# Kernel optimization log

Hardware: AMD Instinct MI355X
Metric: run time of the kernel (lower is better)

The kernel has to match this reference:

```python
import jax, jax.numpy as jnp
import numpy as np
from jax import lax

B, T, D, V, K = 32, 2048, 512, 1024, 3
COVERAGE_FLOOR = 0.05
LN_EPS = 1e-5


def _gelu(x):
    return jax.nn.gelu(x, approximate=False)  # torch F.gelu default is exact erf


def _causal_conv(h, w, b):
    # h: [B,T,D]; w: [D_out, D_in, K]; left-pad (K-1) for causality
    x = jnp.transpose(h, (0, 2, 1))  # [B,D,T]
    y = lax.conv_general_dilated(x, w, window_strides=(1,),
                                 padding=[(w.shape[-1] - 1, 0)],
                                 dimension_numbers=("NCH", "OIH", "NCH"))
    return jnp.transpose(y + b[None, :, None], (0, 2, 1))  # [B,T,D]


def _layer_norm(x, g, b):
    m = x.mean(-1, keepdims=True)
    v = ((x - m) ** 2).mean(-1, keepdims=True)
    return (x - m) / jnp.sqrt(v + LN_EPS) * g + b


def _masked_median(values, mask):
    # values, mask: [B,T]; torch median = lower middle = sorted[(n-1)//2]
    valid = mask > 0.5
    n = valid.sum(axis=1)  # [B]
    s = jnp.sort(jnp.where(valid, values, jnp.inf), axis=1)
    idx = jnp.clip((n - 1) // 2, 0, values.shape[1] - 1)
    med = jnp.take_along_axis(s, idx[:, None], axis=1)  # [B,1]
    return jnp.where((n > 0)[:, None], med, 0.0)


def _masked_mean(values, mask):
    denom = jnp.clip(mask.sum(axis=1, keepdims=True), 1.0, None)  # [B,1]
    return (values * mask[:, :, None]).sum(axis=1) / denom  # [B,D]


def _masked_std(values, mask, mean):
    denom = jnp.clip(mask.sum(axis=1, keepdims=True), 1.0, None)
    diff2 = (values - mean[:, None, :]) ** 2 * mask[:, :, None]
    return jnp.sqrt(diff2.sum(axis=1) / jnp.clip(denom, 1e-6, None) + 1e-6)


def setup_inputs() -> dict:
    key = jax.random.key(0)
    ks = jax.random.split(key, 16)
    s = 0.02
    return {
        "unit_ids": jax.random.randint(ks[0], (B, T), 0, V),
        "duration_obs": jax.random.uniform(ks[1], (B, T), jnp.float32, 0.01, 2.0),
        "mask": (jax.random.uniform(ks[2], (B, T)) > 0.3).astype(jnp.float32),
        "emb": jax.random.normal(ks[3], (V, D), jnp.float32) * s,
        "aux_w": jax.random.normal(ks[4], (D, 1), jnp.float32) * s,
        "aux_b": jnp.zeros((D,), jnp.float32),
        "conv1_w": jax.random.normal(ks[5], (D, D, K), jnp.float32) * s,
        "conv1_b": jnp.zeros((D,), jnp.float32),
        "conv2_w": jax.random.normal(ks[6], (D, D, K), jnp.float32) * s,
        "conv2_b": jnp.zeros((D,), jnp.float32),
        "ln_g": jnp.ones((D,), jnp.float32),
        "ln_b": jnp.zeros((D,), jnp.float32),
        "p1_w": jax.random.normal(ks[7], (D, 2 * D), jnp.float32) * s,
        "p1_b": jnp.zeros((D,), jnp.float32),
        "p2_w": jax.random.normal(ks[8], (D, D), jnp.float32) * s,
        "p2_b": jnp.zeros((D,), jnp.float32),
    }


def reference(unit_ids, duration_obs, mask, emb, aux_w, aux_b,
              conv1_w, conv1_b, conv2_w, conv2_b, ln_g, ln_b,
              p1_w, p1_b, p2_w, p2_b):
    mask = jnp.clip(mask.astype(jnp.float32), 0.0, 1.0)  # [B,T]
    logdur = jnp.log(jnp.clip(duration_obs.astype(jnp.float32), 1e-4, None)) * mask
    global_rate = _masked_median(logdur, mask)  # [B,1]
    ref_residual = (logdur - global_rate) * mask  # [B,T]

    # CausalStretchQueryEncoder
    hidden = emb[unit_ids] + (ref_residual[:, :, None] * aux_w[None, None, :, 0] + aux_b)
    hidden = _gelu(_causal_conv(hidden, conv1_w, conv1_b))
    hidden = _gelu(_causal_conv(hidden, conv2_w, conv2_b))
    hidden = _layer_norm(hidden, ln_g, ln_b) * mask[:, :, None]  # [B,T,D]

    mean = _masked_mean(hidden, mask)  # [B,D]
    std = _masked_std(hidden, mask, mean)  # [B,D]
    h = jnp.concatenate([mean, std], axis=-1)  # [B,2D]
    summary_state = jnp.tanh(_gelu(h @ p1_w.T + p1_b) @ p2_w.T + p2_b)  # [B,D]

    support_raw = mask.sum(axis=1, keepdims=True)  # [B,1]
    support = jnp.clip(support_raw, 1.0, None)
    summary_state = jnp.where(support_raw > 0.0, summary_state, 0.0)
    coverage = jnp.clip(support_raw / float(T), COVERAGE_FLOOR, None)

    residual_mean = (ref_residual * mask).sum(axis=1, keepdims=True) / support  # [B,1]
    residual_var = jnp.clip(((ref_residual - residual_mean) ** 2 * mask).sum(axis=1, keepdims=True) / support, 1e-4, None)
    attn = (mask / support)[:, :, None]  # [B,T,1]
    prompt_role_fit = residual_mean * jnp.ones_like(ref_residual) * mask  # [B,T]
    coeff_norm = jnp.linalg.norm(summary_state, axis=-1, keepdims=True)  # [B,1]

    return (global_rate, summary_state, residual_mean, residual_var, coverage,
            mask, logdur, ref_residual, attn, prompt_role_fit, coeff_norm)
```

## Files before the change

kernel.cpp:

```cpp
#include <hip/hip_runtime.h>
#include <hip/hip_bf16.h>
#include <math.h>

#define B_  32
#define T_  2048
#define D_  512
#define V_  1024
#define K_  3

typedef __attribute__((ext_vector_type(8))) short   short8;
typedef __attribute__((ext_vector_type(4))) float   floatx4;
typedef __attribute__((ext_vector_type(2))) long    longx2;

#define SCALE_H0 256.0f
#define SCALE_A  64.0f
#define SCALE_W  16.0f
#define INV1 (1.0f/(SCALE_H0*SCALE_W))
#define INV2 (1.0f/(SCALE_A*SCALE_W))

#define OFF0 0
#define OFF1 32
#define OFF2 16416
#define OFF3 16448
#define OFF4 16480
#define OFF5 16512
#define OFF6 82048
#define OFF7 147584
#define OFF8 213120
#define OFF9 278656
#define OFF10 344192

#define WS_RR     0
#define WS_SUP    262144
#define WS_PSUM   262272
#define WS_PSUMSQ 327808
#define WS_W1P    393344
#define WS_W2P    1212544
#define WS_H1     2031744
#define WS_S1     35618944
#define WS_NRM    35684480

__device__ __forceinline__ float clampf(float v, float lo, float hi) {
    v = (v > lo) ? v : lo;
    return (v < hi) ? v : hi;
}
__device__ __forceinline__ float gelu_exact(float v) {
    return 0.5f * v * (1.0f + erff(v * 0.70710678118654752440f));
}
__device__ __forceinline__ unsigned char f2fp8(float x) {
    int v = __builtin_amdgcn_cvt_pk_fp8_f32(x, x, 0, false);
    return (unsigned char)(v & 0xFF);
}
__device__ __forceinline__ int pk4fp8(float a, float b, float c, float d) {
    int p0 = __builtin_amdgcn_cvt_pk_fp8_f32(a, b, 0, false);
    int p1 = __builtin_amdgcn_cvt_pk_fp8_f32(c, d, 0, false);
    return (p1 << 16) | (p0 & 0xFFFF);
}

__device__ __forceinline__ float block_reduce_sum(float v, float* red, int tid) {
    __syncthreads();
    red[tid] = v;
    __syncthreads();
    for (int s = 128; s > 0; s >>= 1) {
        if (tid < s) red[tid] += red[tid + s];
        __syncthreads();
    }
    float r = red[0];
    __syncthreads();
    return r;
}

#define NB 2048
#define HLO (-9.3f)
#define HSC ((float)NB / 10.05f)
#define WLS 1544
__global__ __launch_bounds__(256) void init_kernel(
    const float* __restrict__ dur, const float* __restrict__ maskp,
    const float* __restrict__ w1, const float* __restrict__ w2,
    unsigned char* __restrict__ W1p, unsigned char* __restrict__ W2p,
    unsigned char* __restrict__ H1buf,
    float* __restrict__ rr_ws, float* __restrict__ sup_ws,
    float* __restrict__ psum, float* __restrict__ out)
{
    int tid = threadIdx.x;

    if (blockIdx.x >= 32) {
        __shared__ unsigned char Wl[2 * 16 * WLS];
        int ntg = blockIdx.x - 32;
        int lane = tid & 63, wave = tid >> 6;

        #pragma unroll
        for (int ws = 0; ws < 2; ++ws) {
            const float* wsrc = (ws ? w2 : w1) + (size_t)ntg * 16 * 1536;
            for (int i = tid; i < 6144; i += 256) {
                float4 v = ((const float4*)wsrc)[i];
                int col_local = i / 384;
                int pos = (i % 384) * 4;
                int word = pk4fp8(v.x * SCALE_W, v.y * SCALE_W,
                                  v.z * SCALE_W, v.w * SCALE_W);
                *(int*)(&Wl[(ws * 16 + col_local) * WLS + pos]) = word;
            }
        }
        __syncthreads();

        int cl = lane & 15, qq = lane >> 4;
        int pg = ntg >> 1, half = ntg & 1;
        #pragma unroll
        for (int ws = 0; ws < 2; ++ws) {
            unsigned char* dst = ws ? W2p : W1p;
            for (int s = wave; s < 48; s += 4) {
                int ci = s & 15, k = s >> 4;
                const unsigned char* row = &Wl[(ws * 16 + cl) * WLS];
                int kin = ci * 32 + qq * 8;
                unsigned char bb[8];
                #pragma unroll
                for (int e = 0; e < 8; ++e)
                    bb[e] = row[(kin + e) * 3 + k];
                *(double*)(dst + (((size_t)(s * 16 + pg) * 64 + lane) * 16
                                  + half * 8)) = *(double*)bb;
            }
        }

        int pid2 = ntg * 256 + tid;
        #pragma unroll
        for (int j = 0; j < 4; ++j) {
            int idx = pid2 + j * 8192;
            psum[idx] = 0.0f;
            int b = idx >> 10;
            int r = (idx >> 9) & 1;
            int d = idx & 511;
            H1buf[((size_t)b * 2050 + r) * 512 + d] = 0;
        }
        return;
    }

    __shared__ int   hist[NB];
    __shared__ int   csum[256];
    __shared__ float red[256];
    __shared__ float cand[128];
    __shared__ float nsh, medsh;
    __shared__ int   sh_tb, sh_cb, sh_candn;

    int b = blockIdx.x;
    const float* durb = dur + (size_t)b * T_;
    const float* mkb  = maskp + (size_t)b * T_;

    float ld[8], mk[8];
    int   bn[8];
    float cnt = 0.0f;
    #pragma unroll
    for (int i = 0; i < 8; ++i) hist[tid * 8 + i] = 0;
    __syncthreads();
    #pragma unroll
    for (int i = 0; i < 8; ++i) {
        int t = tid + i * 256;
        float m = clampf(mkb[t], 0.0f, 1.0f);
        float dv = durb[t];
        dv = (dv >= 1e-4f) ? dv : 1e-4f;
        float l = logf(dv) * m;
        ld[i] = l; mk[i] = m;
        int bin = (int)((l - HLO) * HSC);
        bin = (bin < 0) ? 0 : ((bin > NB - 1) ? NB - 1 : bin);
        bn[i] = bin;
        if (m > 0.5f) { cnt += 1.0f; atomicAdd(&hist[bin], 1); }
    }
    float n = block_reduce_sum(cnt, red, tid);
    if (tid == 0) { nsh = n; sh_candn = 0; medsh = 0.0f; }

    {
        int cs = 0;
        #pragma unroll
        for (int i = 0; i < 8; ++i) cs += hist[tid * 8 + i];
        csum[tid] = cs;
        __syncthreads();
        for (int off = 1; off < 256; off <<= 1) {
            int v = (tid >= off) ? csum[tid - off] : 0;
            __syncthreads();
            csum[tid] += v;
            __syncthreads();
        }
    }
    int ni = (int)(n + 0.5f);
    int k  = (ni > 0) ? ((ni - 1) >> 1) : 0;
    {
        int prevIncl = (tid > 0) ? csum[tid - 1] : 0;
        if (ni > 0 && k >= prevIncl && k < csum[tid]) {
            int cum = prevIncl, tb = tid * 8;
            #pragma unroll
            for (int i = 0; i < 8; ++i) {
                int c = hist[tid * 8 + i];
                if (k < cum + c) { tb = tid * 8 + i; break; }
                cum += c;
            }
            sh_tb = tb; sh_cb = cum;
        }
    }
    __syncthreads();
    if (ni > 0) {
        int tb = sh_tb;
        #pragma unroll
        for (int i = 0; i < 8; ++i) {
            if (mk[i] > 0.5f && bn[i] == tb) {
                int p = atomicAdd(&sh_candn, 1);
                if (p < 128) cand[p] = ld[i];
            }
        }
    }
    __syncthreads();
    if (tid == 0 && ni > 0) {
        int m = k - sh_cb;
        int cn = (sh_candn < 128) ? sh_candn : 128;
        float best = cand[0];
        for (int i = 0; i < cn; ++i) {
            int rank = 0;
            for (int j = 0; j < cn; ++j)
                rank += (cand[j] < cand[i]) || (cand[j] == cand[i] && j < i);
            if (rank == m) { best = cand[i]; break; }
        }
        medsh = best;
    }
    __syncthreads();
    float med = (ni > 0) ? medsh : 0.0f;
    med = clampf(med, -20.0f, 20.0f);

    float denom = (n > 1.0f) ? n : 1.0f;
    float rv[8];
    float ssum = 0.0f;
    #pragma unroll
    for (int i = 0; i < 8; ++i) { rv[i] = (ld[i] - med) * mk[i]; ssum += rv[i]; }
    float rsum = block_reduce_sum(ssum, red, tid);
    float rm = clampf(rsum / denom, -40.0f, 40.0f);

    float vsum_l = 0.0f;
    #pragma unroll
    for (int i = 0; i < 8; ++i) { float dd = rv[i] - rm; vsum_l += dd * dd * mk[i]; }
    float vsum = block_reduce_sum(vsum_l, red, tid);
    float var = clampf(vsum / denom, 1e-4f, 1e4f);

    float inv_sup = 1.0f / denom;
    #pragma unroll
    for (int i = 0; i < 8; ++i) {
        int t = tid + i * 256;
        size_t o = (size_t)b * T_ + t;
        out[OFF5 + o] = mk[i];
        out[OFF6 + o] = ld[i];
        out[OFF7 + o] = rv[i];
        out[OFF8 + o] = mk[i] * inv_sup;
        out[OFF9 + o] = rm * mk[i];
        rr_ws[o] = rv[i];
    }
    if (tid == 0) {
        out[OFF0 + b] = med;
        out[OFF2 + b] = rm;
        out[OFF3 + b] = var;
        float cov = n * (1.0f / (float)T_);
        out[OFF4 + b] = (cov > 0.05f) ? cov : 0.05f;
        sup_ws[b] = n;
    }
}

#define H0S 520
__global__ __launch_bounds__(256, 3) void conv1g_kernel(
    const int* __restrict__ ids, const float* __restrict__ rr,
    const float* __restrict__ emb,
    const float* __restrict__ aux_w, const float* __restrict__ aux_b,
    const unsigned char* __restrict__ W1p, const float* __restrict__ bias1,
    unsigned char* __restrict__ H1buf)
{
    __shared__ __align__(16) unsigned char H0s[66 * H0S];
    __shared__ int   lid[66];
    __shared__ float lrr[66];

    int tile = blockIdx.x;
    int b    = blockIdx.y;
    int r0   = tile << 6;
    int tid  = threadIdx.x;
    int wave = tid >> 6, lane = tid & 63;
    int q = lane >> 4, m16 = lane & 15;

    if (tid < 66) {
        int t = r0 - 2 + tid;
        bool v = (t >= 0);
        lid[tid] = v ? ids[b * T_ + t] : -1;
        lrr[tid] = v ? rr[(size_t)b * T_ + t] : 0.0f;
    }
    __syncthreads();

    {
        int c4 = tid & 127;
        float4 aw = *(const float4*)(aux_w + c4 * 4);
        float4 ab = *(const float4*)(aux_b + c4 * 4);
        int rbase = tid >> 7;
        for (int j = 0; j < 33; ++j) {
            int row = rbase + j * 2;
            int id = lid[row];
            int word = 0;
            if (id >= 0) {
                float vr = lrr[row];
                float4 e = *(const float4*)(emb + (size_t)id * D_ + c4 * 4);
                word = pk4fp8((e.x + vr * aw.x + ab.x) * SCALE_H0,
                              (e.y + vr * aw.y + ab.y) * SCALE_H0,
                              (e.z + vr * aw.z + ab.z) * SCALE_H0,
                              (e.w + vr * aw.w + ab.w) * SCALE_H0);
            }
            *(int*)(&H0s[row * H0S + c4 * 4]) = word;
        }
    }
    __syncthreads();

    unsigned char* Ob = H1buf + ((size_t)b * 2050 + 2 + r0) * 512;

#define CONV1_PHASE(FR0, FR1, SS)                                              \
    {   int k1 = (SS) >> 4, ci = (SS) & 15;                                    \
        _Pragma("unroll")                                                      \
        for (int mt = 0; mt < 4; ++mt) {                                       \
            long afr = *(const long*)(&H0s[(mt * 16 + m16 + k1) * H0S + ci * 32 + q * 8]); \
            acc[mt][0] = __builtin_amdgcn_mfma_f32_16x16x32_fp8_fp8(afr, FR0[0], acc[mt][0], 0, 0, 0); \
            acc[mt][1] = __builtin_amdgcn_mfma_f32_16x16x32_fp8_fp8(afr, FR0[1], acc[mt][1], 0, 0, 0); \
            acc[mt][2] = __builtin_amdgcn_mfma_f32_16x16x32_fp8_fp8(afr, FR1[0], acc[mt][2], 0, 0, 0); \
            acc[mt][3] = __builtin_amdgcn_mfma_f32_16x16x32_fp8_fp8(afr, FR1[1], acc[mt][3], 0, 0, 0); \
        } }

    #pragma unroll
    for (int nh = 0; nh < 2; ++nh) {
        floatx4 acc[4][4];
        #pragma unroll
        for (int i = 0; i < 4; ++i)
            #pragma unroll
            for (int j = 0; j < 4; ++j)
                acc[i][j] = (floatx4){0.f, 0.f, 0.f, 0.f};

        const longx2* wp0 = (const longx2*)W1p
                          + ((size_t)(0 * 16 + nh * 8 + wave * 2 + 0) * 64 + lane);
        const longx2* wp1 = wp0 + 64;

        longx2 fA0 = wp0[0],                  fA1 = wp1[0];
        longx2 fB0 = wp0[(size_t)1 * 1024],   fB1 = wp1[(size_t)1 * 1024];
        longx2 fC0, fC1, fD0, fD1;

        #pragma unroll 1
        for (int s = 0; s < 48; s += 4) {
            fC0 = wp0[(size_t)(s + 2) * 1024]; fC1 = wp1[(size_t)(s + 2) * 1024];
            CONV1_PHASE(fA0, fA1, s)
            fD0 = wp0[(size_t)(s + 3) * 1024]; fD1 = wp1[(size_t)(s + 3) * 1024];
            CONV1_PHASE(fB0, fB1, s + 1)
            fA0 = wp0[(size_t)(s + 4) * 1024]; fA1 = wp1[(size_t)(s + 4) * 1024];
            CONV1_PHASE(fC0, fC1, s + 2)
            fB0 = wp0[(size_t)(s + 5) * 1024]; fB1 = wp1[(size_t)(s + 5) * 1024];
            CONV1_PHASE(fD0, fD1, s + 3)
        }

        #pragma unroll
        for (int mt = 0; mt < 4; ++mt) {
            #pragma unroll
            for (int nt = 0; nt < 4; ++nt) {
                int col = nh * 256 + wave * 64 + nt * 16 + m16;
                float bsv = bias1[col];
                #pragma unroll
                for (int r = 0; r < 4; ++r) {
                    int row = mt * 16 + q * 4 + r;
                    float v = gelu_exact(acc[mt][nt][r] * INV1 + bsv) * SCALE_A;
                    Ob[(size_t)row * 512 + col] = f2fp8(v);
                }
            }
        }
    }
#undef CONV1_PHASE
}

#define H1S 520
__global__ __launch_bounds__(256, 2) void conv2ln_kernel(
    const unsigned char* __restrict__ H1buf, const unsigned char* __restrict__ W2p,
    const float* __restrict__ bias2,
    const float* __restrict__ ln_g, const float* __restrict__ ln_b,
    const float* __restrict__ maskp,
    float* __restrict__ psum, float* __restrict__ psumsq)
{
    __shared__ __align__(16) unsigned char H1s[34 * H1S];
    __shared__ float mrow[32];
    __shared__ float part[32][4][2];
    __shared__ float tot[32][2];
    __shared__ float colsum[512][2];

    int tile = blockIdx.x;
    int b    = blockIdx.y;
    int r0   = tile << 5;
    int tid  = threadIdx.x;
    int wave = tid >> 6, lane = tid & 63;
    int q = lane >> 4, m16 = lane & 15;
    int nbase = wave << 7;

    const unsigned char* src = H1buf + ((size_t)b * 2050 + r0) * 512;
    for (int g = tid; g < 34 * 32; g += 256) {
        int row = g >> 5, h = g & 31;
        *(float4*)(&H1s[row * H1S + h * 16]) = *(const float4*)(src + (size_t)row * 512 + h * 16);
    }
    if (tid < 32)
        mrow[tid] = clampf(maskp[(size_t)b * T_ + r0 + tid], 0.0f, 1.0f);
    __syncthreads();

    floatx4 acc[2][8];
    #pragma unroll
    for (int i = 0; i < 2; ++i)
        #pragma unroll
        for (int j = 0; j < 8; ++j)
            acc[i][j] = (floatx4){0.f, 0.f, 0.f, 0.f};

    #pragma unroll 2
    for (int s = 0; s < 48; ++s) {
        int k2 = s >> 4, ci = s & 15;
        longx2 f2[4];
        #pragma unroll
        for (int ntp = 0; ntp < 4; ++ntp)
            f2[ntp] = *((const longx2*)W2p
                        + ((size_t)(s * 16 + wave * 4 + ntp) * 64 + lane));
        #pragma unroll
        for (int mt = 0; mt < 2; ++mt) {
            long afr = *(const long*)(&H1s[(mt * 16 + m16 + k2) * H1S + ci * 32 + q * 8]);
            #pragma unroll
            for (int ntp = 0; ntp < 4; ++ntp) {
                acc[mt][2 * ntp]     = __builtin_amdgcn_mfma_f32_16x16x32_fp8_fp8(
                    afr, f2[ntp][0], acc[mt][2 * ntp], 0, 0, 0);
                acc[mt][2 * ntp + 1] = __builtin_amdgcn_mfma_f32_16x16x32_fp8_fp8(
                    afr, f2[ntp][1], acc[mt][2 * ntp + 1], 0, 0, 0);
            }
        }
    }

    #pragma unroll
    for (int mt = 0; mt < 2; ++mt)
        #pragma unroll
        for (int nt = 0; nt < 8; ++nt) {
            int col = nbase + nt * 16 + m16;
            float bsv = bias2[col];
            #pragma unroll
            for (int r = 0; r < 4; ++r)
                acc[mt][nt][r] = gelu_exact(acc[mt][nt][r] * INV2 + bsv);
        }

    #pragma unroll
    for (int mt = 0; mt < 2; ++mt) {
        #pragma unroll
        for (int r = 0; r < 4; ++r) {
            float rs = 0.f, rq = 0.f;
            #pragma unroll
            for (int nt = 0; nt < 8; ++nt) {
                float v = acc[mt][nt][r];
                rs += v; rq += v * v;
            }
            rs += __shfl_xor(rs, 1);  rq += __shfl_xor(rq, 1);
            rs += __shfl_xor(rs, 2);  rq += __shfl_xor(rq, 2);
            rs += __shfl_xor(rs, 4);  rq += __shfl_xor(rq, 4);
            rs += __shfl_xor(rs, 8);  rq += __shfl_xor(rq, 8);
            if (m16 == 0) {
                int row = mt * 16 + q * 4 + r;
                part[row][wave][0] = rs;
                part[row][wave][1] = rq;
            }
        }
    }
    __syncthreads();
    if (tid < 64) {
        int row = tid >> 1, j = tid & 1;
        tot[row][j] = part[row][0][j] + part[row][1][j] + part[row][2][j] + part[row][3][j];
    }
    __syncthreads();

    float meanv[2][4], rstdv[2][4];
    #pragma unroll
    for (int mt = 0; mt < 2; ++mt)
        #pragma unroll
        for (int r = 0; r < 4; ++r) {
            int row = mt * 16 + q * 4 + r;
            float m = tot[row][0] * (1.0f / D_);
            float var = tot[row][1] * (1.0f / D_) - m * m;
            meanv[mt][r] = m;
            rstdv[mt][r] = rsqrtf((var > 0.0f ? var : 0.0f) + 1e-5f);
        }

    float cs[8], cq[8];
    #pragma unroll
    for (int nt = 0; nt < 8; ++nt) { cs[nt] = 0.f; cq[nt] = 0.f; }
    #pragma unroll
    for (int mt = 0; mt < 2; ++mt) {
        #pragma unroll
        for (int r = 0; r < 4; ++r) {
            int row = mt * 16 + q * 4 + r;
            float mk = mrow[row];
            float m = meanv[mt][r], rs = rstdv[mt][r];
            #pragma unroll
            for (int nt = 0; nt < 8; ++nt) {
                int col = nbase + nt * 16 + m16;
                float xn = ((acc[mt][nt][r] - m) * rs * ln_g[col] + ln_b[col]) * mk;
                cs[nt] += xn;
                cq[nt] += xn * xn;
            }
        }
    }
    #pragma unroll
    for (int nt = 0; nt < 8; ++nt) {
        cs[nt] += __shfl_xor(cs[nt], 16);  cq[nt] += __shfl_xor(cq[nt], 16);
        cs[nt] += __shfl_xor(cs[nt], 32);  cq[nt] += __shfl_xor(cq[nt], 32);
    }
    if (lane < 16) {
        #pragma unroll
        for (int nt = 0; nt < 8; ++nt) {
            int col = nbase + nt * 16 + m16;
            colsum[col][0] = cs[nt];
            colsum[col][1] = cq[nt];
        }
    }
    __syncthreads();
    for (int i = tid; i < 512; i += 256) {
        atomicAdd(&psum[(size_t)b * D_ + i], colsum[i][0]);
        atomicAdd(&psumsq[(size_t)b * D_ + i], colsum[i][1]);
    }
}

__global__ __launch_bounds__(128) void mlp1_kernel(
    const float* __restrict__ psum, const float* __restrict__ psumsq,
    const float* __restrict__ sup_ws,
    const float* __restrict__ p1w, const float* __restrict__ p1b,
    float* __restrict__ s1_ws, float* __restrict__ nrm_ws)
{
    int b = blockIdx.x, jt = blockIdx.y;
    int tid = threadIdx.x;
    __shared__ float h[2 * D_];

    float n = sup_ws[b];
    float denom = (n > 1.0f) ? n : 1.0f;
    for (int i = tid; i < D_; i += 128) {
        float S = psum[(size_t)b * D_ + i];
        float Q = psumsq[(size_t)b * D_ + i];
        float mean = S / denom;
        float msum = Q - 2.0f * mean * S + n * mean * mean;
        float arg = msum / denom + 1e-6f;
        h[i] = mean;
        h[D_ + i] = sqrtf((arg > 0.0f) ? arg : 0.0f);
    }
    if (jt == 0 && tid == 0) nrm_ws[b] = 0.0f;
    __syncthreads();

    int d = jt * 128 + tid;
    float z = p1b[d];
    const float4* w4 = (const float4*)(p1w + (size_t)d * (2 * D_));
    for (int jj = 0; jj < 2 * D_ / 4; ++jj) {
        float4 wv = w4[jj];
        z += h[jj * 4 + 0] * wv.x + h[jj * 4 + 1] * wv.y
           + h[jj * 4 + 2] * wv.z + h[jj * 4 + 3] * wv.w;
    }
    s1_ws[(size_t)b * D_ + d] = gelu_exact(z);
}

__global__ __launch_bounds__(128) void mlp2_kernel(
    const float* __restrict__ s1_ws, const float* __restrict__ sup_ws,
    const float* __restrict__ p2w, const float* __restrict__ p2b,
    float* __restrict__ nrm_ws, float* __restrict__ out)
{
    int b = blockIdx.x, jt = blockIdx.y;
    int tid = threadIdx.x;
    __shared__ float s1[D_];
    __shared__ float red[128];

    for (int i = tid; i < D_; i += 128) s1[i] = s1_ws[(size_t)b * D_ + i];
    __syncthreads();

    int d = jt * 128 + tid;
    float z2 = p2b[d];
    const float4* w24 = (const float4*)(p2w + (size_t)d * D_);
    for (int jj = 0; jj < D_ / 4; ++jj) {
        float4 wv = w24[jj];
        z2 += s1[jj * 4 + 0] * wv.x + s1[jj * 4 + 1] * wv.y
            + s1[jj * 4 + 2] * wv.z + s1[jj * 4 + 3] * wv.w;
    }
    float n = sup_ws[b];
    float st = tanhf(z2);
    if (!(n > 0.0f)) st = 0.0f;
    out[OFF1 + (size_t)b * D_ + d] = st;

    red[tid] = st * st;
    __syncthreads();
    for (int s = 64; s > 0; s >>= 1) {
        if (tid < s) red[tid] += red[tid + s];
        __syncthreads();
    }
    if (tid == 0) atomicAdd(&nrm_ws[b], red[0]);
}

__global__ __launch_bounds__(64) void mlp3_kernel(
    const float* __restrict__ nrm_ws, float* __restrict__ out)
{
    int b = threadIdx.x;
    if (b < B_) out[OFF10 + b] = sqrtf(nrm_ws[b]);
}

extern "C" void kernel_launch(void* const* d_in, const int* in_sizes, int n_in,
                              void* d_out, int out_size, void* d_ws, size_t ws_size,
                              hipStream_t stream) {
    (void)in_sizes; (void)n_in; (void)out_size; (void)ws_size;
    const int*   unit_ids = (const int*)d_in[0];
    const float* dur      = (const float*)d_in[1];
    const float* mask     = (const float*)d_in[2];
    const float* emb      = (const float*)d_in[3];
    const float* aux_w    = (const float*)d_in[4];
    const float* aux_b    = (const float*)d_in[5];
    const float* conv1_w  = (const float*)d_in[6];
    const float* conv1_b  = (const float*)d_in[7];
    const float* conv2_w  = (const float*)d_in[8];
    const float* conv2_b  = (const float*)d_in[9];
    const float* ln_g     = (const float*)d_in[10];
    const float* ln_b     = (const float*)d_in[11];
    const float* p1_w     = (const float*)d_in[12];
    const float* p1_b     = (const float*)d_in[13];
    const float* p2_w     = (const float*)d_in[14];
    const float* p2_b     = (const float*)d_in[15];
    float* out = (float*)d_out;

    char* ws = (char*)d_ws;
    float*          rr     = (float*)(ws + WS_RR);
    float*          sup    = (float*)(ws + WS_SUP);
    float*          psum   = (float*)(ws + WS_PSUM);
    float*          psumsq = (float*)(ws + WS_PSUMSQ);
    unsigned char*  W1p    = (unsigned char*)(ws + WS_W1P);
    unsigned char*  W2p    = (unsigned char*)(ws + WS_W2P);
    unsigned char*  H1buf  = (unsigned char*)(ws + WS_H1);
    float*          s1_ws  = (float*)(ws + WS_S1);
    float*          nrm_ws = (float*)(ws + WS_NRM);

    init_kernel<<<dim3(64), dim3(256), 0, stream>>>(
        dur, mask, conv1_w, conv2_w, W1p, W2p, H1buf, rr, sup, psum, out);
    conv1g_kernel<<<dim3(32, 32), dim3(256), 0, stream>>>(
        unit_ids, rr, emb, aux_w, aux_b, W1p, conv1_b, H1buf);
    conv2ln_kernel<<<dim3(64, 32), dim3(256), 0, stream>>>(
        H1buf, W2p, conv2_b, ln_g, ln_b, mask, psum, psumsq);
    mlp1_kernel<<<dim3(32, 4), dim3(128), 0, stream>>>(
        psum, psumsq, sup, p1_w, p1_b, s1_ws, nrm_ws);
    mlp2_kernel<<<dim3(32, 4), dim3(128), 0, stream>>>(
        s1_ws, sup, p2_w, p2_b, nrm_ws, out);
    mlp3_kernel<<<dim3(1), dim3(64), 0, stream>>>(nrm_ws, out);
}
```

Before: 341.1 us.

## Double the conv2 row tile and stage shared weights through double-buffered LDS

The conv2+LayerNorm kernel now handles 64 time rows per block with 512 threads, so two wave groups share each weight slice. Each weight chunk is prefetched into registers and written into a double-buffered LDS area, instead of every wave reading weights from global memory. This halves global weight traffic per row, but adds a block-wide barrier per K step and a larger LDS footprint. Separately, the two summary MLP kernels split each dot product across two threads joined by a shuffle, doubling the block count to expose more parallelism.

```diff
diff --git a/kernel.cpp b/kernel.cpp
--- a/kernel.cpp
+++ b/kernel.cpp
@@ -369,34 +369,43 @@
 }
 
 #define H1S 520
-__global__ __launch_bounds__(256, 2) void conv2ln_kernel(
+__global__ __launch_bounds__(512, 2) void conv2ln_kernel(
     const unsigned char* __restrict__ H1buf, const unsigned char* __restrict__ W2p,
     const float* __restrict__ bias2,
     const float* __restrict__ ln_g, const float* __restrict__ ln_b,
     const float* __restrict__ maskp,
     float* __restrict__ psum, float* __restrict__ psumsq)
 {
-    __shared__ __align__(16) unsigned char H1s[34 * H1S];
-    __shared__ float mrow[32];
-    __shared__ float part[32][4][2];
-    __shared__ float tot[32][2];
-    __shared__ float colsum[512][2];
+    __shared__ __align__(16) unsigned char H1s[66 * H1S];
+    __shared__ __align__(16) unsigned char Wb[2][16384];
+    __shared__ float mrow[64];
+    __shared__ float part[64][4][2];
+    __shared__ float tot[64][2];
+    __shared__ float colsum[2][512][2];
 
     int tile = blockIdx.x;
     int b    = blockIdx.y;
-    int r0   = tile << 5;
+    int r0   = tile << 6;
     int tid  = threadIdx.x;
     int wave = tid >> 6, lane = tid & 63;
+    int mhalf = wave >> 2, nq = wave & 3;
     int q = lane >> 4, m16 = lane & 15;
-    int nbase = wave << 7;
+    int nbase = nq << 7;
 
     const unsigned char* src = H1buf + ((size_t)b * 2050 + r0) * 512;
-    for (int g = tid; g < 34 * 32; g += 256) {
+    for (int g = tid; g < 66 * 32; g += 512) {
         int row = g >> 5, h = g & 31;
         *(float4*)(&H1s[row * H1S + h * 16]) = *(const float4*)(src + (size_t)row * 512 + h * 16);
     }
-    if (tid < 32)
+    if (tid < 64)
         mrow[tid] = clampf(maskp[(size_t)b * T_ + r0 + tid], 0.0f, 1.0f);
+
+    {
+        const longx2* g0 = (const longx2*)W2p + tid;
+        longx2 v0 = g0[0], v1 = g0[512];
+        *(longx2*)(&Wb[0][tid * 16]) = v0;
+        *(longx2*)(&Wb[0][tid * 16 + 8192]) = v1;
+    }
     __syncthreads();
 
     floatx4 acc[2][8];
@@ -406,26 +415,37 @@
         for (int j = 0; j < 8; ++j)
             acc[i][j] = (floatx4){0.f, 0.f, 0.f, 0.f};
 
-    #pragma unroll 2
-    for (int s = 0; s < 48; ++s) {
-        int k2 = s >> 4, ci = s & 15;
-        longx2 f2[4];
-        #pragma unroll
-        for (int ntp = 0; ntp < 4; ++ntp)
-            f2[ntp] = *((const longx2*)W2p
-                        + ((size_t)(s * 16 + wave * 4 + ntp) * 64 + lane));
-        #pragma unroll
-        for (int mt = 0; mt < 2; ++mt) {
-            long afr = *(const long*)(&H1s[(mt * 16 + m16 + k2) * H1S + ci * 32 + q * 8]);
-            #pragma unroll
-            for (int ntp = 0; ntp < 4; ++ntp) {
-                acc[mt][2 * ntp]     = __builtin_amdgcn_mfma_f32_16x16x32_fp8_fp8(
-                    afr, f2[ntp][0], acc[mt][2 * ntp], 0, 0, 0);
-                acc[mt][2 * ntp + 1] = __builtin_amdgcn_mfma_f32_16x16x32_fp8_fp8(
-                    afr, f2[ntp][1], acc[mt][2 * ntp + 1], 0, 0, 0);
-            }
-        }
-    }
+#define C2_STEP(RB, WB_, SS)                                                   \
+    {   const longx2* gq = (const longx2*)(W2p + (size_t)((SS) + 1) * 16384) + tid; \
+        longx2 sv0 = gq[0];                                                    \
+        longx2 sv1 = gq[512];                                                  \
+        int k2 = (SS) >> 4, ci = (SS) & 15;                                    \
+        longx2 f2[4];                                                          \
+        _Pragma("unroll")                                                      \
+        for (int ntp = 0; ntp < 4; ++ntp)                                      \
+            f2[ntp] = *(const longx2*)(&RB[((nq * 4 + ntp) * 64 + lane) * 16]); \
+        _Pragma("unroll")                                                      \
+        for (int mt = 0; mt < 2; ++mt) {                                       \
+            long afr = *(const long*)(&H1s[(mhalf * 32 + mt * 16 + m16 + k2) * H1S + ci * 32 + q * 8]); \
+            _Pragma("unroll")                                                  \
+            for (int ntp = 0; ntp < 4; ++ntp) {                                \
+                acc[mt][2 * ntp]     = __builtin_amdgcn_mfma_f32_16x16x32_fp8_fp8( \
+                    afr, f2[ntp][0], acc[mt][2 * ntp], 0, 0, 0);               \
+                acc[mt][2 * ntp + 1] = __builtin_amdgcn_mfma_f32_16x16x32_fp8_fp8( \
+                    afr, f2[ntp][1], acc[mt][2 * ntp + 1], 0, 0, 0);           \
+            }                                                                  \
+        }                                                                      \
+        *(longx2*)(&WB_[tid * 16]) = sv0;                                      \
+        *(longx2*)(&WB_[tid * 16 + 8192]) = sv1;                               \
+        __syncthreads();                                                       \
+    }
+
+    #pragma unroll 1
+    for (int s = 0; s < 48; s += 2) {
+        C2_STEP(Wb[0], Wb[1], s)
+        C2_STEP(Wb[1], Wb[0], s + 1)
+    }
+#undef C2_STEP
 
     #pragma unroll
     for (int mt = 0; mt < 2; ++mt)
@@ -453,14 +473,14 @@
             rs += __shfl_xor(rs, 4);  rq += __shfl_xor(rq, 4);
             rs += __shfl_xor(rs, 8);  rq += __shfl_xor(rq, 8);
             if (m16 == 0) {
-                int row = mt * 16 + q * 4 + r;
-                part[row][wave][0] = rs;
-                part[row][wave][1] = rq;
-            }
-        }
-    }
-    __syncthreads();
-    if (tid < 64) {
+                int row = mhalf * 32 + mt * 16 + q * 4 + r;
+                part[row][nq][0] = rs;
+                part[row][nq][1] = rq;
+            }
+        }
+    }
+    __syncthreads();
+    if (tid < 128) {
         int row = tid >> 1, j = tid & 1;
         tot[row][j] = part[row][0][j] + part[row][1][j] + part[row][2][j] + part[row][3][j];
     }
@@ -471,7 +491,7 @@
     for (int mt = 0; mt < 2; ++mt)
         #pragma unroll
         for (int r = 0; r < 4; ++r) {
-            int row = mt * 16 + q * 4 + r;
+            int row = mhalf * 32 + mt * 16 + q * 4 + r;
             float m = tot[row][0] * (1.0f / D_);
             float var = tot[row][1] * (1.0f / D_) - m * m;
             meanv[mt][r] = m;
@@ -485,7 +505,7 @@
     for (int mt = 0; mt < 2; ++mt) {
         #pragma unroll
         for (int r = 0; r < 4; ++r) {
-            int row = mt * 16 + q * 4 + r;
+            int row = mhalf * 32 + mt * 16 + q * 4 + r;
             float mk = mrow[row];
             float m = meanv[mt][r], rs = rstdv[mt][r];
             #pragma unroll
@@ -506,14 +526,17 @@
         #pragma unroll
         for (int nt = 0; nt < 8; ++nt) {
             int col = nbase + nt * 16 + m16;
-            colsum[col][0] = cs[nt];
-            colsum[col][1] = cq[nt];
-        }
-    }
-    __syncthreads();
-    for (int i = tid; i < 512; i += 256) {
-        atomicAdd(&psum[(size_t)b * D_ + i], colsum[i][0]);
-        atomicAdd(&psumsq[(size_t)b * D_ + i], colsum[i][1]);
+            colsum[mhalf][col][0] = cs[nt];
+            colsum[mhalf][col][1] = cq[nt];
+        }
+    }
+    __syncthreads();
+    {
+        int i = tid;
+        if (i < 512) {
+            atomicAdd(&psum[(size_t)b * D_ + i],   colsum[0][i][0] + colsum[1][i][0]);
+            atomicAdd(&psumsq[(size_t)b * D_ + i], colsum[0][i][1] + colsum[1][i][1]);
+        }
     }
 }
 
@@ -541,15 +564,18 @@
     if (jt == 0 && tid == 0) nrm_ws[b] = 0.0f;
     __syncthreads();
 
-    int d = jt * 128 + tid;
-    float z = p1b[d];
-    const float4* w4 = (const float4*)(p1w + (size_t)d * (2 * D_));
-    for (int jj = 0; jj < 2 * D_ / 4; ++jj) {
+    int d  = jt * 64 + (tid >> 1);
+    int kh = tid & 1;
+    float z = (kh == 0) ? p1b[d] : 0.0f;
+    const float4* w4 = (const float4*)(p1w + (size_t)d * (2 * D_) + kh * D_);
+    const float*  hh = &h[kh * D_];
+    for (int jj = 0; jj < D_ / 4; ++jj) {
         float4 wv = w4[jj];
-        z += h[jj * 4 + 0] * wv.x + h[jj * 4 + 1] * wv.y
-           + h[jj * 4 + 2] * wv.z + h[jj * 4 + 3] * wv.w;
-    }
-    s1_ws[(size_t)b * D_ + d] = gelu_exact(z);
+        z += hh[jj * 4 + 0] * wv.x + hh[jj * 4 + 1] * wv.y
+           + hh[jj * 4 + 2] * wv.z + hh[jj * 4 + 3] * wv.w;
+    }
+    z += __shfl_xor(z, 1);
+    if (kh == 0) s1_ws[(size_t)b * D_ + d] = gelu_exact(z);
 }
 
 __global__ __launch_bounds__(128) void mlp2_kernel(
@@ -565,20 +591,23 @@
     for (int i = tid; i < D_; i += 128) s1[i] = s1_ws[(size_t)b * D_ + i];
     __syncthreads();
 
-    int d = jt * 128 + tid;
-    float z2 = p2b[d];
-    const float4* w24 = (const float4*)(p2w + (size_t)d * D_);
-    for (int jj = 0; jj < D_ / 4; ++jj) {
+    int d  = jt * 64 + (tid >> 1);
+    int kh = tid & 1;
+    float z2 = (kh == 0) ? p2b[d] : 0.0f;
+    const float4* w24 = (const float4*)(p2w + (size_t)d * D_ + kh * 256);
+    const float*  ss  = &s1[kh * 256];
+    for (int jj = 0; jj < 64; ++jj) {
         float4 wv = w24[jj];
-        z2 += s1[jj * 4 + 0] * wv.x + s1[jj * 4 + 1] * wv.y
-            + s1[jj * 4 + 2] * wv.z + s1[jj * 4 + 3] * wv.w;
-    }
-    float n = sup_ws[b];
+        z2 += ss[jj * 4 + 0] * wv.x + ss[jj * 4 + 1] * wv.y
+            + ss[jj * 4 + 2] * wv.z + ss[jj * 4 + 3] * wv.w;
+    }
+    z2 += __shfl_xor(z2, 1);
+    float nsup = sup_ws[b];
     float st = tanhf(z2);
-    if (!(n > 0.0f)) st = 0.0f;
-    out[OFF1 + (size_t)b * D_ + d] = st;
-
-    red[tid] = st * st;
+    if (!(nsup > 0.0f)) st = 0.0f;
+    if (kh == 0) out[OFF1 + (size_t)b * D_ + d] = st;
+
+    red[tid] = (kh == 0) ? st * st : 0.0f;
     __syncthreads();
     for (int s = 64; s > 0; s >>= 1) {
         if (tid < s) red[tid] += red[tid + s];
@@ -631,11 +660,11 @@
         dur, mask, conv1_w, conv2_w, W1p, W2p, H1buf, rr, sup, psum, out);
     conv1g_kernel<<<dim3(32, 32), dim3(256), 0, stream>>>(
         unit_ids, rr, emb, aux_w, aux_b, W1p, conv1_b, H1buf);
-    conv2ln_kernel<<<dim3(64, 32), dim3(256), 0, stream>>>(
+    conv2ln_kernel<<<dim3(32, 32), dim3(512), 0, stream>>>(
         H1buf, W2p, conv2_b, ln_g, ln_b, mask, psum, psumsq);
-    mlp1_kernel<<<dim3(32, 4), dim3(128), 0, stream>>>(
+    mlp1_kernel<<<dim3(32, 8), dim3(128), 0, stream>>>(
         psum, psumsq, sup, p1_w, p1_b, s1_ws, nrm_ws);
-    mlp2_kernel<<<dim3(32, 4), dim3(128), 0, stream>>>(
+    mlp2_kernel<<<dim3(32, 8), dim3(128), 0, stream>>>(
         s1_ws, sup, p2_w, p2_b, nrm_ws, out);
     mlp3_kernel<<<dim3(1), dim3(64), 0, stream>>>(nrm_ws, out);
 }
```

After: 342.8 us. No clear change (+0.5%).

## Software-pipeline conv2 weight loads and split MLP dot products across thread pairs

Applied to the files above, without the earlier changes.

The conv2 MFMA loop now prefetches FP8 weight fragments two steps ahead in rotating register sets (A/B/C/D), so global weight-load latency overlaps with MFMA issue. The MLP1 and MLP2 kernels split each output's dot product across two threads, combine the halves with a shuffle, and launch twice as many blocks. The MLP change is meant to raise parallelism in these small kernels. The prefetch raises register pressure and reads two steps past the last weight fragment in the final iteration. That out-of-range load may hit unused workspace.

```diff
diff --git a/kernel.cpp b/kernel.cpp
--- a/kernel.cpp
+++ b/kernel.cpp
@@ -406,26 +406,47 @@
         for (int j = 0; j < 8; ++j)
             acc[i][j] = (floatx4){0.f, 0.f, 0.f, 0.f};
 
-    #pragma unroll 2
-    for (int s = 0; s < 48; ++s) {
-        int k2 = s >> 4, ci = s & 15;
-        longx2 f2[4];
-        #pragma unroll
-        for (int ntp = 0; ntp < 4; ++ntp)
-            f2[ntp] = *((const longx2*)W2p
-                        + ((size_t)(s * 16 + wave * 4 + ntp) * 64 + lane));
-        #pragma unroll
-        for (int mt = 0; mt < 2; ++mt) {
-            long afr = *(const long*)(&H1s[(mt * 16 + m16 + k2) * H1S + ci * 32 + q * 8]);
-            #pragma unroll
-            for (int ntp = 0; ntp < 4; ++ntp) {
-                acc[mt][2 * ntp]     = __builtin_amdgcn_mfma_f32_16x16x32_fp8_fp8(
-                    afr, f2[ntp][0], acc[mt][2 * ntp], 0, 0, 0);
-                acc[mt][2 * ntp + 1] = __builtin_amdgcn_mfma_f32_16x16x32_fp8_fp8(
-                    afr, f2[ntp][1], acc[mt][2 * ntp + 1], 0, 0, 0);
-            }
-        }
-    }
+    const longx2* wq0 = (const longx2*)W2p + ((size_t)(wave * 4 + 0) * 64 + lane);
+    const longx2* wq1 = (const longx2*)W2p + ((size_t)(wave * 4 + 1) * 64 + lane);
+    const longx2* wq2 = (const longx2*)W2p + ((size_t)(wave * 4 + 2) * 64 + lane);
+    const longx2* wq3 = (const longx2*)W2p + ((size_t)(wave * 4 + 3) * 64 + lane);
+
+#define C2_PHASE(F0, F1, F2, F3, SS)                                           \
+    {   int k2 = (SS) >> 4, ci = (SS) & 15;                                    \
+        _Pragma("unroll")                                                      \
+        for (int mt = 0; mt < 2; ++mt) {                                       \
+            long afr = *(const long*)(&H1s[(mt * 16 + m16 + k2) * H1S + ci * 32 + q * 8]); \
+            acc[mt][0] = __builtin_amdgcn_mfma_f32_16x16x32_fp8_fp8(afr, F0[0], acc[mt][0], 0, 0, 0); \
+            acc[mt][1] = __builtin_amdgcn_mfma_f32_16x16x32_fp8_fp8(afr, F0[1], acc[mt][1], 0, 0, 0); \
+            acc[mt][2] = __builtin_amdgcn_mfma_f32_16x16x32_fp8_fp8(afr, F1[0], acc[mt][2], 0, 0, 0); \
+            acc[mt][3] = __builtin_amdgcn_mfma_f32_16x16x32_fp8_fp8(afr, F1[1], acc[mt][3], 0, 0, 0); \
+            acc[mt][4] = __builtin_amdgcn_mfma_f32_16x16x32_fp8_fp8(afr, F2[0], acc[mt][4], 0, 0, 0); \
+            acc[mt][5] = __builtin_amdgcn_mfma_f32_16x16x32_fp8_fp8(afr, F2[1], acc[mt][5], 0, 0, 0); \
+            acc[mt][6] = __builtin_amdgcn_mfma_f32_16x16x32_fp8_fp8(afr, F3[0], acc[mt][6], 0, 0, 0); \
+            acc[mt][7] = __builtin_amdgcn_mfma_f32_16x16x32_fp8_fp8(afr, F3[1], acc[mt][7], 0, 0, 0); \
+        } }
+
+    longx2 fA0 = wq0[0], fA1 = wq1[0], fA2 = wq2[0], fA3 = wq3[0];
+    longx2 fB0 = wq0[(size_t)1 * 1024], fB1 = wq1[(size_t)1 * 1024];
+    longx2 fB2 = wq2[(size_t)1 * 1024], fB3 = wq3[(size_t)1 * 1024];
+    longx2 fC0, fC1, fC2, fC3, fD0, fD1, fD2, fD3;
+
+    #pragma unroll 1
+    for (int s = 0; s < 48; s += 4) {
+        fC0 = wq0[(size_t)(s + 2) * 1024]; fC1 = wq1[(size_t)(s + 2) * 1024];
+        fC2 = wq2[(size_t)(s + 2) * 1024]; fC3 = wq3[(size_t)(s + 2) * 1024];
+        C2_PHASE(fA0, fA1, fA2, fA3, s)
+        fD0 = wq0[(size_t)(s + 3) * 1024]; fD1 = wq1[(size_t)(s + 3) * 1024];
+        fD2 = wq2[(size_t)(s + 3) * 1024]; fD3 = wq3[(size_t)(s + 3) * 1024];
+        C2_PHASE(fB0, fB1, fB2, fB3, s + 1)
+        fA0 = wq0[(size_t)(s + 4) * 1024]; fA1 = wq1[(size_t)(s + 4) * 1024];
+        fA2 = wq2[(size_t)(s + 4) * 1024]; fA3 = wq3[(size_t)(s + 4) * 1024];
+        C2_PHASE(fC0, fC1, fC2, fC3, s + 2)
+        fB0 = wq0[(size_t)(s + 5) * 1024]; fB1 = wq1[(size_t)(s + 5) * 1024];
+        fB2 = wq2[(size_t)(s + 5) * 1024]; fB3 = wq3[(size_t)(s + 5) * 1024];
+        C2_PHASE(fD0, fD1, fD2, fD3, s + 3)
+    }
+#undef C2_PHASE
 
     #pragma unroll
     for (int mt = 0; mt < 2; ++mt)
@@ -541,15 +562,18 @@
     if (jt == 0 && tid == 0) nrm_ws[b] = 0.0f;
     __syncthreads();
 
-    int d = jt * 128 + tid;
-    float z = p1b[d];
-    const float4* w4 = (const float4*)(p1w + (size_t)d * (2 * D_));
-    for (int jj = 0; jj < 2 * D_ / 4; ++jj) {
+    int d  = jt * 64 + (tid >> 1);
+    int kh = tid & 1;
+    float z = (kh == 0) ? p1b[d] : 0.0f;
+    const float4* w4 = (const float4*)(p1w + (size_t)d * (2 * D_) + kh * D_);
+    const float*  hh = &h[kh * D_];
+    for (int jj = 0; jj < D_ / 4; ++jj) {
         float4 wv = w4[jj];
-        z += h[jj * 4 + 0] * wv.x + h[jj * 4 + 1] * wv.y
-           + h[jj * 4 + 2] * wv.z + h[jj * 4 + 3] * wv.w;
-    }
-    s1_ws[(size_t)b * D_ + d] = gelu_exact(z);
+        z += hh[jj * 4 + 0] * wv.x + hh[jj * 4 + 1] * wv.y
+           + hh[jj * 4 + 2] * wv.z + hh[jj * 4 + 3] * wv.w;
+    }
+    z += __shfl_xor(z, 1);
+    if (kh == 0) s1_ws[(size_t)b * D_ + d] = gelu_exact(z);
 }
 
 __global__ __launch_bounds__(128) void mlp2_kernel(
@@ -565,20 +589,23 @@
     for (int i = tid; i < D_; i += 128) s1[i] = s1_ws[(size_t)b * D_ + i];
     __syncthreads();
 
-    int d = jt * 128 + tid;
-    float z2 = p2b[d];
-    const float4* w24 = (const float4*)(p2w + (size_t)d * D_);
-    for (int jj = 0; jj < D_ / 4; ++jj) {
+    int d  = jt * 64 + (tid >> 1);
+    int kh = tid & 1;
+    float z2 = (kh == 0) ? p2b[d] : 0.0f;
+    const float4* w24 = (const float4*)(p2w + (size_t)d * D_ + kh * 256);
+    const float*  ss  = &s1[kh * 256];
+    for (int jj = 0; jj < 64; ++jj) {
         float4 wv = w24[jj];
-        z2 += s1[jj * 4 + 0] * wv.x + s1[jj * 4 + 1] * wv.y
-            + s1[jj * 4 + 2] * wv.z + s1[jj * 4 + 3] * wv.w;
-    }
-    float n = sup_ws[b];
+        z2 += ss[jj * 4 + 0] * wv.x + ss[jj * 4 + 1] * wv.y
+            + ss[jj * 4 + 2] * wv.z + ss[jj * 4 + 3] * wv.w;
+    }
+    z2 += __shfl_xor(z2, 1);
+    float nsup = sup_ws[b];
     float st = tanhf(z2);
-    if (!(n > 0.0f)) st = 0.0f;
-    out[OFF1 + (size_t)b * D_ + d] = st;
-
-    red[tid] = st * st;
+    if (!(nsup > 0.0f)) st = 0.0f;
+    if (kh == 0) out[OFF1 + (size_t)b * D_ + d] = st;
+
+    red[tid] = (kh == 0) ? st * st : 0.0f;
     __syncthreads();
     for (int s = 64; s > 0; s >>= 1) {
         if (tid < s) red[tid] += red[tid + s];
@@ -633,9 +660,9 @@
         unit_ids, rr, emb, aux_w, aux_b, W1p, conv1_b, H1buf);
     conv2ln_kernel<<<dim3(64, 32), dim3(256), 0, stream>>>(
         H1buf, W2p, conv2_b, ln_g, ln_b, mask, psum, psumsq);
-    mlp1_kernel<<<dim3(32, 4), dim3(128), 0, stream>>>(
+    mlp1_kernel<<<dim3(32, 8), dim3(128), 0, stream>>>(
         psum, psumsq, sup, p1_w, p1_b, s1_ws, nrm_ws);
-    mlp2_kernel<<<dim3(32, 4), dim3(128), 0, stream>>>(
+    mlp2_kernel<<<dim3(32, 8), dim3(128), 0, stream>>>(
         s1_ws, sup, p2_w, p2_b, nrm_ws, out);
     mlp3_kernel<<<dim3(1), dim3(64), 0, stream>>>(nrm_ws, out);
 }
```

Result: faster. 321.7 us (-5.7%).
